# Performance work log

Measured on AMD Instinct MI355X. Metric: run time of the kernel, lower is better.

Reference implementation:

```python
import jax, jax.numpy as jnp
import numpy as np

HSV_BINS = 32
LBP_BINS = 256
NEG_SLOPE = 0.2
ENV_CLASSES = 4
SEASON_CLASSES = 4


def rgb_to_hsv(img):
    # img: [N, 3, H, W] in [0, 1]
    img = jnp.clip(img, 0.0, 1.0)
    r, g, b = img[:, 0], img[:, 1], img[:, 2]
    maxc = img.max(axis=1)
    minc = img.min(axis=1)
    delta = maxc - minc
    mask = delta > 1e-6
    safe = jnp.where(mask, delta, 1.0)
    hue = jnp.zeros_like(maxc)
    hue = jnp.where((maxc == r) & mask, jnp.mod((g - b) / safe, 6.0), hue)
    hue = jnp.where((maxc == g) & mask, (b - r) / safe + 2.0, hue)
    hue = jnp.where((maxc == b) & mask, (r - g) / safe + 4.0, hue)
    hue = hue / 6.0
    sat = jnp.where(maxc > 1e-6, delta / jnp.maximum(maxc, 1e-6), jnp.zeros_like(maxc))
    return jnp.stack((hue, sat, maxc), axis=1)


def hist_features(hsv):
    # torch.histc(bins=32, min=0, max=1); HSV values are all in [0,1],
    # value==1.0 falls into the last bin -> clip(floor(v*bins), 0, bins-1).
    N, C, H, W = hsv.shape
    v = hsv.reshape(N * C, H * W)
    idx = jnp.clip(jnp.floor(v * HSV_BINS).astype(jnp.int32), 0, HSV_BINS - 1)
    offset = jnp.arange(N * C, dtype=jnp.int32)[:, None] * HSV_BINS
    counts = jnp.bincount((idx + offset).reshape(-1), length=N * C * HSV_BINS)
    counts = counts.reshape(N * C, HSV_BINS).astype(jnp.float32)
    counts = counts / jnp.maximum(counts.sum(-1, keepdims=True), 1.0)
    return counts.reshape(N, C * HSV_BINS)


def lbp_features(hsv):
    N, C, H, W = hsv.shape
    p = jnp.pad(hsv, ((0, 0), (0, 0), (1, 1), (1, 1)), mode='reflect')
    offsets = [(0, 0), (0, 1), (0, 2), (1, 2), (2, 2), (2, 1), (2, 0), (1, 0)]
    codes = jnp.zeros((N, C, H, W), dtype=jnp.int32)
    for bit, (dy, dx) in enumerate(offsets):
        nb = jax.lax.dynamic_slice(p, (0, 0, dy, dx), (N, C, H, W))
        codes = codes + (nb >= hsv).astype(jnp.int32) * (1 << bit)
    codes = codes.reshape(N * C, H * W)
    offset = jnp.arange(N * C, dtype=jnp.int32)[:, None] * LBP_BINS
    counts = jnp.bincount((codes + offset).reshape(-1), length=N * C * LBP_BINS)
    counts = counts.reshape(N * C, LBP_BINS).astype(jnp.float32)
    counts = counts / jnp.maximum(counts.sum(-1, keepdims=True), 1.0)
    return counts.reshape(N, C * LBP_BINS)


def setup_inputs() -> dict:
    key = jax.random.key(0)
    k1, k2, k3, k4, k5 = jax.random.split(key, 5)
    B, T, H, W = 4, 8, 512, 512
    sequence = jax.random.uniform(k1, (B, T, 3, H, W), dtype=jnp.float32)
    high = jax.random.normal(k2, (B * T, 2048), dtype=jnp.float32)
    Wp = jax.random.normal(k3, (512, 2912), dtype=jnp.float32) * 0.02
    bp = jnp.zeros((512,), dtype=jnp.float32)
    environment_id = jax.random.randint(k4, (B,), 0, ENV_CLASSES, dtype=jnp.int64 if jax.config.jax_enable_x64 else jnp.int32)
    season_id = jax.random.randint(k5, (B,), 0, SEASON_CLASSES, dtype=jnp.int64 if jax.config.jax_enable_x64 else jnp.int32)
    return {"sequence": sequence, "high": high, "W": Wp, "b": bp,
            "environment_id": environment_id, "season_id": season_id}


def reference(sequence, high, W, b, environment_id, season_id):
    B, T, C, H, Wd = sequence.shape
    # inputs are already in [0,1) so _to_unit_rgb reduces to a clamp
    frames = jnp.clip(sequence, 0.0, 1.0).reshape(B * T, C, H, Wd)
    hsv = rgb_to_hsv(frames)                                   # [BT,3,H,W]
    low = jnp.concatenate((hist_features(hsv), lbp_features(hsv)), axis=1)  # [BT,864]
    fused = jnp.concatenate((high, low), axis=1).reshape(B, T, -1)          # [B,T,2912]
    aggregated = fused.mean(axis=1)                             # [B,2912]
    z = aggregated @ W.T + b                                    # Linear(2912->512)
    c_feat = jnp.where(z >= 0, z, NEG_SLOPE * z)                # LeakyReLU(0.2)
    env = jax.nn.one_hot(environment_id, ENV_CLASSES, dtype=jnp.float32)
    season = jax.nn.one_hot(season_id, SEASON_CLASSES, dtype=jnp.float32)
    c_cls = jnp.concatenate((env, season), axis=1)
    return (c_feat, c_cls)
```

## Files before the change

### kernel.cpp

```cpp
#include <hip/hip_runtime.h>

#define IMH 512
#define IMW 512
#define NFRAMES 32
#define HSV_BINS 32
#define LBP_BINS 256
#define FEAT_HIGH 2048
#define FEAT_LOW (3*HSV_BINS + 3*LBP_BINS)
#define FEAT_TOT (FEAT_HIGH + FEAT_LOW)
#define OUT_COLS 512
#define R_ROWS 4
#define STRIPS (IMH / (4 * R_ROWS))
#define NHREP 16
#define NLREP 4

__device__ __forceinline__ void rgb2hsv(float r, float g, float b,
                                        float& h, float& s, float& v) {
    float maxc = fmaxf(r, fmaxf(g, b));
    float minc = fminf(r, fminf(g, b));
    float delta = maxc - minc;
    bool mask = delta > 1e-6f;
    float rd = __builtin_amdgcn_rcpf(mask ? delta : 1.0f);
    float hue = 0.0f;
    if (mask) {
        if (maxc == r) { float t = (g - b) * rd; hue = (t >= 0.0f) ? t : t + 6.0f; }
        if (maxc == g) hue = (b - r) * rd + 2.0f;
        if (maxc == b) hue = (r - g) * rd + 4.0f;
    }
    h = hue * (1.0f / 6.0f);
    s = (maxc > 1e-6f) ? delta * __builtin_amdgcn_rcpf(maxc) : 0.0f;
    v = maxc;
}

__global__ __launch_bounds__(256, 4) void hist_lbp_kernel(const float* __restrict__ seq,
                                                          unsigned* __restrict__ hist_g,
                                                          unsigned* __restrict__ lbp_g) {
    const int n     = blockIdx.x >> 5;
    const int strip = blockIdx.x & (STRIPS - 1);
    const int tid   = threadIdx.x;
    const int lane  = tid & 63;
    const int w     = tid >> 6;
    const int x0    = lane << 3;
    const int yb    = strip * (4 * R_ROWS) + w * R_ROWS;

    __shared__ unsigned sh_hist[3][NHREP][HSV_BINS + 1];
    __shared__ unsigned sh_lbp[3][NLREP][LBP_BINS + 1];

    for (int i = tid; i < 3 * NHREP * (HSV_BINS + 1); i += 256) ((unsigned*)sh_hist)[i] = 0u;
    for (int i = tid; i < 3 * NLREP * (LBP_BINS + 1); i += 256) ((unsigned*)sh_lbp)[i] = 0u;
    __syncthreads();

    unsigned* hb0 = &sh_hist[0][lane & (NHREP - 1)][0];
    unsigned* hb1 = &sh_hist[1][lane & (NHREP - 1)][0];
    unsigned* hb2 = &sh_hist[2][lane & (NHREP - 1)][0];
    unsigned* lb0 = &sh_lbp[0][lane & (NLREP - 1)][0];
    unsigned* lb1 = &sh_lbp[1][lane & (NLREP - 1)][0];
    unsigned* lb2 = &sh_lbp[2][lane & (NLREP - 1)][0];

    const float* base = seq + (size_t)n * 3 * IMH * IMW;

    float P[3][10];
    float N[3][10];
    int   pc[3][8];

#pragma unroll
    for (int s = 0; s < R_ROWS + 2; ++s) {
        int gy = yb + s - 1;
        gy = (gy < 0) ? 1 : ((gy > IMH - 1) ? IMH - 2 : gy);
        {
            const float* p0 = base + (size_t)gy * IMW + x0;
            float4 ra = *(const float4*)(p0);
            float4 rb = *(const float4*)(p0 + 4);
            float4 ga = *(const float4*)(p0 + IMH * IMW);
            float4 gb = *(const float4*)(p0 + IMH * IMW + 4);
            float4 ba = *(const float4*)(p0 + 2 * IMH * IMW);
            float4 bb = *(const float4*)(p0 + 2 * IMH * IMW + 4);
            float rr[8] = {ra.x, ra.y, ra.z, ra.w, rb.x, rb.y, rb.z, rb.w};
            float gg[8] = {ga.x, ga.y, ga.z, ga.w, gb.x, gb.y, gb.z, gb.w};
            float bv[8] = {ba.x, ba.y, ba.z, ba.w, bb.x, bb.y, bb.z, bb.w};
#pragma unroll
            for (int j = 0; j < 8; ++j)
                rgb2hsv(rr[j], gg[j], bv[j], N[0][j + 1], N[1][j + 1], N[2][j + 1]);
#pragma unroll
            for (int c = 0; c < 3; ++c) {
                float l = __shfl(N[c][8], (lane + 63) & 63);
                float r = __shfl(N[c][1], (lane + 1) & 63);
                N[c][0] = (lane == 0)  ? N[c][2] : l;
                N[c][9] = (lane == 63) ? N[c][7] : r;
            }
        }

        if (s >= 2) {
#pragma unroll
            for (int c = 0; c < 3; ++c) {
                unsigned* hb = (c == 0) ? hb0 : ((c == 1) ? hb1 : hb2);
                unsigned* lb = (c == 0) ? lb0 : ((c == 1) ? lb1 : lb2);
#pragma unroll
                for (int j = 0; j < 8; ++j) {
                    float ce = P[c][j + 1];
                    int code = pc[c][j];
                    code |= (N[c][j + 2] >= ce) ? 16 : 0;
                    code |= (N[c][j + 1] >= ce) ? 32 : 0;
                    code |= (N[c][j]     >= ce) ? 64 : 0;
                    int bin = min((int)(ce * 32.0f), HSV_BINS - 1);
                    atomicAdd(hb + bin, 1u);
                    atomicAdd(lb + code, 1u);
                }
            }
        }

        if (s >= 1 && s <= R_ROWS) {
#pragma unroll
            for (int c = 0; c < 3; ++c) {
#pragma unroll
                for (int j = 0; j < 8; ++j) {
                    float ce = N[c][j + 1];
                    int code = 0;
                    code |= (P[c][j]     >= ce) ? 1   : 0;
                    code |= (P[c][j + 1] >= ce) ? 2   : 0;
                    code |= (P[c][j + 2] >= ce) ? 4   : 0;
                    code |= (N[c][j + 2] >= ce) ? 8   : 0;
                    code |= (N[c][j]     >= ce) ? 128 : 0;
                    pc[c][j] = code;
                }
            }
        }

#pragma unroll
        for (int c = 0; c < 3; ++c)
#pragma unroll
            for (int k = 0; k < 10; ++k) P[c][k] = N[c][k];
    }

    __syncthreads();
    for (int i = tid; i < 3 * HSV_BINS; i += 256) {
        int c = i >> 5, b = i & 31;
        unsigned s = 0;
#pragma unroll
        for (int r = 0; r < NHREP; ++r) s += sh_hist[c][r][b];
        if (s) atomicAdd(&hist_g[n * 3 * HSV_BINS + i], s);
    }
    for (int i = tid; i < 3 * LBP_BINS; i += 256) {
        int c = i >> 8, b = i & 255;
        unsigned s = 0;
#pragma unroll
        for (int r = 0; r < NLREP; ++r) s += sh_lbp[c][r][b];
        if (s) atomicAdd(&lbp_g[n * 3 * LBP_BINS + i], s);
    }
}

__global__ __launch_bounds__(256) void agg_cls_kernel(const float* __restrict__ high,
                                                      const unsigned* __restrict__ hist_g,
                                                      const unsigned* __restrict__ lbp_g,
                                                      const int* __restrict__ env,
                                                      const int* __restrict__ season,
                                                      float* __restrict__ agg,
                                                      float* __restrict__ out) {
    int idx = blockIdx.x * blockDim.x + threadIdx.x;
    if (idx >= 4 * FEAT_TOT + 32) return;
    if (idx >= 4 * FEAT_TOT) {
        int t = idx - 4 * FEAT_TOT;
        int i = t >> 3;
        int p = t & 7;
        float v;
        if (p < 4) v = (env[i] == p) ? 1.0f : 0.0f;
        else       v = (season[i] == p - 4) ? 1.0f : 0.0f;
        out[4 * OUT_COLS + t] = v;
        return;
    }
    int bb = idx / FEAT_TOT;
    int k  = idx % FEAT_TOT;
    float s = 0.0f;
    const float inv = 1.0f / 262144.0f;
    if (k < FEAT_HIGH) {
#pragma unroll
        for (int t = 0; t < 8; t++) s += high[(size_t)(bb * 8 + t) * FEAT_HIGH + k];
    } else if (k < FEAT_HIGH + 3 * HSV_BINS) {
        int f = k - FEAT_HIGH;
#pragma unroll
        for (int t = 0; t < 8; t++)
            s += (float)hist_g[(bb * 8 + t) * 3 * HSV_BINS + f] * inv;
    } else {
        int f = k - FEAT_HIGH - 3 * HSV_BINS;
#pragma unroll
        for (int t = 0; t < 8; t++)
            s += (float)lbp_g[(bb * 8 + t) * 3 * LBP_BINS + f] * inv;
    }
    agg[idx] = s * 0.125f;
}

__global__ __launch_bounds__(256) void gemm_kernel(const float* __restrict__ agg,
                                                   const float* __restrict__ Wm,
                                                   const float* __restrict__ bias,
                                                   float* __restrict__ out) {
    const int j = blockIdx.x;
    const int tid = threadIdx.x;
    const float* wrow = Wm + (size_t)j * FEAT_TOT;
    float a0 = 0.f, a1 = 0.f, a2 = 0.f, a3 = 0.f;
    for (int k = tid; k < FEAT_TOT; k += 256) {
        float w = wrow[k];
        a0 += agg[k] * w;
        a1 += agg[FEAT_TOT + k] * w;
        a2 += agg[2 * FEAT_TOT + k] * w;
        a3 += agg[3 * FEAT_TOT + k] * w;
    }
#pragma unroll
    for (int off = 32; off > 0; off >>= 1) {
        a0 += __shfl_down(a0, off);
        a1 += __shfl_down(a1, off);
        a2 += __shfl_down(a2, off);
        a3 += __shfl_down(a3, off);
    }
    __shared__ float red[4][4];
    if ((tid & 63) == 0) {
        int w = tid >> 6;
        red[w][0] = a0; red[w][1] = a1; red[w][2] = a2; red[w][3] = a3;
    }
    __syncthreads();
    if (tid < 4) {
        float z = red[0][tid] + red[1][tid] + red[2][tid] + red[3][tid] + bias[j];
        out[tid * OUT_COLS + j] = (z >= 0.0f) ? z : 0.2f * z;
    }
}

extern "C" void kernel_launch(void* const* d_in, const int* in_sizes, int n_in,
                              void* d_out, int out_size, void* d_ws, size_t ws_size,
                              hipStream_t stream) {
    const float* seq    = (const float*)d_in[0];
    const float* high   = (const float*)d_in[1];
    const float* Wm     = (const float*)d_in[2];
    const float* bias   = (const float*)d_in[3];
    const int*   env    = (const int*)d_in[4];
    const int*   season = (const int*)d_in[5];
    float* out = (float*)d_out;

    unsigned* hist_g = (unsigned*)d_ws;
    unsigned* lbp_g  = hist_g + NFRAMES * 3 * HSV_BINS;
    float*    agg    = (float*)(lbp_g + NFRAMES * 3 * LBP_BINS);

    size_t histBytes = (size_t)(NFRAMES * 3 * HSV_BINS + NFRAMES * 3 * LBP_BINS) * sizeof(unsigned);
    hipMemsetAsync(d_ws, 0, histBytes, stream);

    hist_lbp_kernel<<<NFRAMES * STRIPS, 256, 0, stream>>>(seq, hist_g, lbp_g);
    agg_cls_kernel<<<(4 * FEAT_TOT + 32 + 255) / 256, 256, 0, stream>>>(high, hist_g, lbp_g, env, season, agg, out);
    gemm_kernel<<<OUT_COLS, 256, 0, stream>>>(agg, Wm, bias, out);
}
```

Before: 192.8 us.

## Prefetch next row, load halo pixels directly, keep three-row HSV window

The row loop is restructured so that the next row's RGB data is loaded into a double buffer while the current row is converted to HSV. Cross-lane shuffles for the left and right halo are replaced by direct scalar global loads of the neighbouring pixels, which are then converted to HSV redundantly. The split partial-code scheme becomes a rotating three-row window that computes the full 8-bit LBP code at once. Occupancy is lowered to 3 waves per SIMD to make room for the extra registers, trading latency hiding through occupancy for explicit prefetch, with 25% more HSV conversions.

```diff
diff --git a/kernel.cpp b/kernel.cpp
--- a/kernel.cpp
+++ b/kernel.cpp
@@ -32,7 +32,7 @@
     v = maxc;
 }
 
-__global__ __launch_bounds__(256, 4) void hist_lbp_kernel(const float* __restrict__ seq,
+__global__ __launch_bounds__(256, 3) void hist_lbp_kernel(const float* __restrict__ seq,
                                                           unsigned* __restrict__ hist_g,
                                                           unsigned* __restrict__ lbp_g) {
     const int n     = blockIdx.x >> 5;
@@ -50,86 +50,80 @@
     for (int i = tid; i < 3 * NLREP * (LBP_BINS + 1); i += 256) ((unsigned*)sh_lbp)[i] = 0u;
     __syncthreads();
 
-    unsigned* hb0 = &sh_hist[0][lane & (NHREP - 1)][0];
-    unsigned* hb1 = &sh_hist[1][lane & (NHREP - 1)][0];
-    unsigned* hb2 = &sh_hist[2][lane & (NHREP - 1)][0];
-    unsigned* lb0 = &sh_lbp[0][lane & (NLREP - 1)][0];
-    unsigned* lb1 = &sh_lbp[1][lane & (NLREP - 1)][0];
-    unsigned* lb2 = &sh_lbp[2][lane & (NLREP - 1)][0];
+    unsigned* hbp[3] = {&sh_hist[0][lane & (NHREP - 1)][0],
+                        &sh_hist[1][lane & (NHREP - 1)][0],
+                        &sh_hist[2][lane & (NHREP - 1)][0]};
+    unsigned* lbp[3] = {&sh_lbp[0][lane & (NLREP - 1)][0],
+                        &sh_lbp[1][lane & (NLREP - 1)][0],
+                        &sh_lbp[2][lane & (NLREP - 1)][0]};
 
     const float* base = seq + (size_t)n * 3 * IMH * IMW;
-
-    float P[3][10];
-    float N[3][10];
-    int   pc[3][8];
-
-#pragma unroll
-    for (int s = 0; s < R_ROWS + 2; ++s) {
+    const int xl = (x0 == 0) ? 1 : x0 - 1;
+    const int xr = (lane == 63) ? IMW - 2 : x0 + 8;
+
+    float rawr[2][10], rawg[2][10], rawb[2][10];
+    float win[3][3][10];
+
+    auto load_row = [&](int s, int bufi) {
         int gy = yb + s - 1;
         gy = (gy < 0) ? 1 : ((gy > IMH - 1) ? IMH - 2 : gy);
-        {
-            const float* p0 = base + (size_t)gy * IMW + x0;
-            float4 ra = *(const float4*)(p0);
-            float4 rb = *(const float4*)(p0 + 4);
-            float4 ga = *(const float4*)(p0 + IMH * IMW);
-            float4 gb = *(const float4*)(p0 + IMH * IMW + 4);
-            float4 ba = *(const float4*)(p0 + 2 * IMH * IMW);
-            float4 bb = *(const float4*)(p0 + 2 * IMH * IMW + 4);
-            float rr[8] = {ra.x, ra.y, ra.z, ra.w, rb.x, rb.y, rb.z, rb.w};
-            float gg[8] = {ga.x, ga.y, ga.z, ga.w, gb.x, gb.y, gb.z, gb.w};
-            float bv[8] = {ba.x, ba.y, ba.z, ba.w, bb.x, bb.y, bb.z, bb.w};
-#pragma unroll
-            for (int j = 0; j < 8; ++j)
-                rgb2hsv(rr[j], gg[j], bv[j], N[0][j + 1], N[1][j + 1], N[2][j + 1]);
+        const float* p0 = base + (size_t)gy * IMW;
+        const float* pr = p0 + x0;
+        float4 ra = *(const float4*)(pr);
+        float4 rb = *(const float4*)(pr + 4);
+        float4 ga = *(const float4*)(pr + IMH * IMW);
+        float4 gb = *(const float4*)(pr + IMH * IMW + 4);
+        float4 ba = *(const float4*)(pr + 2 * IMH * IMW);
+        float4 bb = *(const float4*)(pr + 2 * IMH * IMW + 4);
+        rawr[bufi][0] = p0[xl];               rawr[bufi][9] = p0[xr];
+        rawg[bufi][0] = p0[IMH * IMW + xl];   rawg[bufi][9] = p0[IMH * IMW + xr];
+        rawb[bufi][0] = p0[2 * IMH * IMW + xl]; rawb[bufi][9] = p0[2 * IMH * IMW + xr];
+        rawr[bufi][1] = ra.x; rawr[bufi][2] = ra.y; rawr[bufi][3] = ra.z; rawr[bufi][4] = ra.w;
+        rawr[bufi][5] = rb.x; rawr[bufi][6] = rb.y; rawr[bufi][7] = rb.z; rawr[bufi][8] = rb.w;
+        rawg[bufi][1] = ga.x; rawg[bufi][2] = ga.y; rawg[bufi][3] = ga.z; rawg[bufi][4] = ga.w;
+        rawg[bufi][5] = gb.x; rawg[bufi][6] = gb.y; rawg[bufi][7] = gb.z; rawg[bufi][8] = gb.w;
+        rawb[bufi][1] = ba.x; rawb[bufi][2] = ba.y; rawb[bufi][3] = ba.z; rawb[bufi][4] = ba.w;
+        rawb[bufi][5] = bb.x; rawb[bufi][6] = bb.y; rawb[bufi][7] = bb.z; rawb[bufi][8] = bb.w;
+    };
+
+    load_row(0, 0);
+#pragma unroll
+    for (int s = 0; s < R_ROWS + 2; ++s) {
+        if (s < R_ROWS + 1) load_row(s + 1, (s + 1) & 1);
+
+        const int ph = s % 3;
+        const int bi = s & 1;
+#pragma unroll
+        for (int j = 0; j < 10; ++j)
+            rgb2hsv(rawr[bi][j], rawg[bi][j], rawb[bi][j],
+                    win[ph][0][j], win[ph][1][j], win[ph][2][j]);
+
+        if (s >= 2) {
+            const int up = (s - 2) % 3;
+            const int cp = (s - 1) % 3;
+            const int dn = ph;
 #pragma unroll
             for (int c = 0; c < 3; ++c) {
-                float l = __shfl(N[c][8], (lane + 63) & 63);
-                float r = __shfl(N[c][1], (lane + 1) & 63);
-                N[c][0] = (lane == 0)  ? N[c][2] : l;
-                N[c][9] = (lane == 63) ? N[c][7] : r;
-            }
-        }
-
-        if (s >= 2) {
-#pragma unroll
-            for (int c = 0; c < 3; ++c) {
-                unsigned* hb = (c == 0) ? hb0 : ((c == 1) ? hb1 : hb2);
-                unsigned* lb = (c == 0) ? lb0 : ((c == 1) ? lb1 : lb2);
+                unsigned* hb = hbp[c];
+                unsigned* lb = lbp[c];
 #pragma unroll
                 for (int j = 0; j < 8; ++j) {
-                    float ce = P[c][j + 1];
-                    int code = pc[c][j];
-                    code |= (N[c][j + 2] >= ce) ? 16 : 0;
-                    code |= (N[c][j + 1] >= ce) ? 32 : 0;
-                    code |= (N[c][j]     >= ce) ? 64 : 0;
+                    float ce = win[cp][c][j + 1];
+                    int code = 0;
+                    code |= (win[up][c][j]     >= ce) ? 1   : 0;
+                    code |= (win[up][c][j + 1] >= ce) ? 2   : 0;
+                    code |= (win[up][c][j + 2] >= ce) ? 4   : 0;
+                    code |= (win[cp][c][j + 2] >= ce) ? 8   : 0;
+                    code |= (win[dn][c][j + 2] >= ce) ? 16  : 0;
+                    code |= (win[dn][c][j + 1] >= ce) ? 32  : 0;
+                    code |= (win[dn][c][j]     >= ce) ? 64  : 0;
+                    code |= (win[cp][c][j]     >= ce) ? 128 : 0;
                     int bin = min((int)(ce * 32.0f), HSV_BINS - 1);
                     atomicAdd(hb + bin, 1u);
                     atomicAdd(lb + code, 1u);
                 }
             }
         }
-
-        if (s >= 1 && s <= R_ROWS) {
-#pragma unroll
-            for (int c = 0; c < 3; ++c) {
-#pragma unroll
-                for (int j = 0; j < 8; ++j) {
-                    float ce = N[c][j + 1];
-                    int code = 0;
-                    code |= (P[c][j]     >= ce) ? 1   : 0;
-                    code |= (P[c][j + 1] >= ce) ? 2   : 0;
-                    code |= (P[c][j + 2] >= ce) ? 4   : 0;
-                    code |= (N[c][j + 2] >= ce) ? 8   : 0;
-                    code |= (N[c][j]     >= ce) ? 128 : 0;
-                    pc[c][j] = code;
-                }
-            }
-        }
-
-#pragma unroll
-        for (int c = 0; c < 3; ++c)
-#pragma unroll
-            for (int k = 0; k < 10; ++k) P[c][k] = N[c][k];
     }
 
     __syncthreads();
```

After: 184.6 us. -4.3%, faster.
